# Optimization experiments

Measured on AMD Instinct MI355X. Metric: run time of the kernel, lower is better.

Reference implementation:

```python
import jax, jax.numpy as jnp
import numpy as np

GAMMA_MIN, GAMMA_MAX = 0.15, 1.0
ALPHA_CAP = 1.0
EPS_L2 = 1e-8
EPS_RMS = 1e-6


def _rmsnorm(x, w):
    return x * jax.lax.rsqrt(jnp.mean(x * x, axis=-1, keepdims=True) + EPS_RMS) * w


def _l2norm(x):
    n = jnp.linalg.norm(x, axis=-1, keepdims=True)
    return x / jnp.maximum(n, EPS_L2)


def _causal_conv(h, kernel):
    # depthwise-shared causal conv over time: out[b,t] = sum_j kernel[j] * h[b, t-j]
    K = kernel.shape[0]
    S = h.shape[1]
    hp = jnp.pad(h, ((0, 0), (K - 1, 0), (0, 0)))
    out = jnp.zeros_like(h)
    for j in range(K):  # K is a small fixed constant (4)
        out = out + kernel[j] * hp[:, K - 1 - j:K - 1 - j + S, :]
    return out


def setup_inputs() -> dict:
    B, S, D, R, K = 8, 1024, 1024, 16, 4
    key = jax.random.key(0)
    ks = jax.random.split(key, 8)
    return {
        'h': jax.random.normal(ks[0], (B, S, D), dtype=jnp.float32),
        'u': jax.random.normal(ks[1], (D, R), dtype=jnp.float32) * 0.05,
        'v': jax.random.normal(ks[2], (D, R), dtype=jnp.float32) * 0.05,
        'decay_logit': jnp.zeros((R,), jnp.float32),
        'alpha_logit': jnp.zeros((R,), jnp.float32),
        'k_base_gate_logit': jnp.float32(0.0),
        'k_base_kernel': jax.random.normal(ks[3], (K,), dtype=jnp.float32) * 0.05,
        'proj_w': jax.random.normal(ks[4], (D, D), dtype=jnp.float32) * 0.02,
        'proj_b': jnp.zeros((D,), jnp.float32),
        'norm1_w': jnp.ones((D,), jnp.float32),
        'norm2_w': jnp.ones((D,), jnp.float32),
        'mlp_w1': jax.random.normal(ks[5], (D, 4 * D), dtype=jnp.float32) * 0.02,
        'mlp_b1': jnp.zeros((4 * D,), jnp.float32),
        'mlp_w2': jax.random.normal(ks[6], (4 * D, D), dtype=jnp.float32) * 0.02,
        'mlp_b2': jnp.zeros((D,), jnp.float32),
    }


def reference(h, u, v, decay_logit, alpha_logit, k_base_gate_logit, k_base_kernel,
              proj_w, proj_b, norm1_w, norm2_w, mlp_w1, mlp_b1, mlp_w2, mlp_b2):
    B, S, D = h.shape
    R = u.shape[1]
    residual = h
    h_norm = _rmsnorm(h, norm1_w)

    # conv k_base term, gated
    gate = jax.nn.sigmoid(k_base_gate_logit)
    out = gate * _causal_conv(h_norm, k_base_kernel)

    # low-rank q/k projections
    alpha = ALPHA_CAP * jax.nn.sigmoid(alpha_logit)  # [R]
    qk = h_norm @ jnp.concatenate((u, v), axis=1)    # [B,S,2R]
    q_raw, k_raw = qk[..., :R], qk[..., R:]
    q = _l2norm(q_raw)
    k = _l2norm(k_raw)

    # per-rank causal decay matrix: w[r,i,j] = gamma[r]^(i-j) for i>=j else 0
    gamma = jnp.clip(jax.nn.sigmoid(decay_logit), GAMMA_MIN, GAMMA_MAX)  # [R]
    pos = jnp.arange(S, dtype=h.dtype)
    diff = jnp.maximum(pos[:, None] - pos[None, :], 0.0)   # [S,S]
    mask = jnp.tril(jnp.ones((S, S), dtype=h.dtype))
    w = (gamma[:, None, None] ** diff) * mask              # [R,S,S]

    q_alpha = q * alpha                                    # [B,S,R]
    A = jnp.einsum('bir,bjr,rij->bij', q_alpha, k, w)      # [B,S,S]
    decay_out = jnp.einsum('bij,bjd->bid', A, h_norm)      # [B,S,D]

    out = out + decay_out
    out = out @ proj_w.T + proj_b
    h2 = residual + out
    hn2 = _rmsnorm(h2, norm2_w)
    mlp_out = jax.nn.gelu(hn2 @ mlp_w1 + mlp_b1) @ mlp_w2 + mlp_b2
    return h2 + mlp_out
```

## Files before the change

### kernel.cpp

```cpp
#include <hip/hip_runtime.h>
#include <hip/hip_bf16.h>
#include <cstdint>
#include <cstddef>

typedef __bf16 bf16;
typedef __bf16 bf16x2 __attribute__((ext_vector_type(2)));
typedef __bf16 bf16x4 __attribute__((ext_vector_type(4)));
typedef __bf16 bf16x8 __attribute__((ext_vector_type(8)));
typedef float  floatx4 __attribute__((ext_vector_type(4)));

#define BB 8
#define SS 1024
#define DD 1024
#define RR 16
#define CHK 64
#define NCH 16

#define PP_ALPHA 0
#define PP_GAMMA 16
#define PP_GP    32
#define PP_KKER  (32 + 16*72)
#define PP_FLOATS 2048

__device__ __forceinline__ float sigmoidf_(float x) { return 1.0f / (1.0f + __expf(-x)); }

__device__ __forceinline__ float gelu_f(float x) {
    float u = 0.7978845608028654f * (x + 0.044715f * x * x * x);
    float t = 1.0f - 2.0f / (__expf(2.0f * u) + 1.0f);
    return 0.5f * x * (1.0f + t);
}

__device__ __forceinline__ void g2l16(const bf16* g, bf16* l) {
    __builtin_amdgcn_global_load_lds(
        (const __attribute__((address_space(1))) void*)g,
        (__attribute__((address_space(3))) void*)l, 16, 0, 0);
}

__global__ void params_kernel(const float* __restrict__ decay_logit,
                              const float* __restrict__ alpha_logit,
                              const float* __restrict__ gate_logit,
                              const float* __restrict__ kbase,
                              float* __restrict__ pp) {
    int t = threadIdx.x;
    if (t < 16) {
        pp[PP_ALPHA + t] = sigmoidf_(alpha_logit[t]);
        float g = sigmoidf_(decay_logit[t]);
        g = fminf(fmaxf(g, 0.15f), 1.0f);
        pp[PP_GAMMA + t] = g;
        float acc = 1.0f;
        for (int p = 0; p < 72; ++p) { pp[PP_GP + t * 72 + p] = acc; acc *= g; }
    }
    if (t >= 16 && t < 20) {
        float gate = sigmoidf_(gate_logit[0]);
        pp[PP_KKER + (t - 16)] = gate * kbase[t - 16];
    }
}

__global__ void uvt_kernel(const float* __restrict__ u, const float* __restrict__ v,
                           bf16* __restrict__ Ut) {
    int c = blockIdx.x;
    const float* src = (c < 16) ? u : v;
    int cc = c & 15;
    for (int d = threadIdx.x; d < 1024; d += 256)
        Ut[c * 1024 + d] = (bf16)src[d * 16 + cc];
}

__global__ __launch_bounds__(256) void rmsrow_kernel(
    const float* __restrict__ x, const float* __restrict__ nw, bf16* __restrict__ y) {
    __shared__ float red[4];
    int t = threadIdx.x;
    size_t row = blockIdx.x;
    float4 hv = ((const float4*)(x + row * DD))[t];
    float ss = hv.x*hv.x + hv.y*hv.y + hv.z*hv.z + hv.w*hv.w;
    for (int m = 32; m; m >>= 1) ss += __shfl_xor(ss, m);
    if ((t & 63) == 0) red[t >> 6] = ss;
    __syncthreads();
    float tot = red[0] + red[1] + red[2] + red[3];
    float rinv = rsqrtf(tot * (1.0f / 1024.0f) + 1e-6f);
    float4 wv = ((const float4*)nw)[t];
    bf16x4 o = { (bf16)(hv.x * rinv * wv.x), (bf16)(hv.y * rinv * wv.y),
                 (bf16)(hv.z * rinv * wv.z), (bf16)(hv.w * rinv * wv.w) };
    ((bf16x4*)(y + row * DD))[t] = o;
}

__global__ __launch_bounds__(256) void qk_kernel(
    const bf16* __restrict__ hn, const bf16* __restrict__ Ut,
    const float* __restrict__ pp, float* __restrict__ qa, float* __restrict__ kk) {
    __shared__ __attribute__((aligned(16))) bf16 As[128 * 64];
    __shared__ __attribute__((aligned(16))) bf16 Bs[32 * 64];
    int tid = threadIdx.x, lane = tid & 63, wid = tid >> 6;
    int quad = lane >> 4, l16 = lane & 15;
    int m0 = blockIdx.x * 128;
    int wm = wid * 32;
    const bf16* Ap[4]; int lo[4];
    #pragma unroll
    for (int j = 0; j < 4; ++j) {
        int s = j * 256 + tid;
        int row = s >> 3, cc = s & 7;
        int gc = cc ^ (row & 7);
        Ap[j] = hn + (size_t)(m0 + row) * DD + gc * 8;
        lo[j] = s * 8;
    }
    int bs_row = tid >> 3, bs_cc = tid & 7;
    int bs_gc = bs_cc ^ (bs_row & 7);
    const bf16* Bp = Ut + (size_t)bs_row * DD + bs_gc * 8;
    int blo = tid * 8;
    floatx4 acc[2][2] = {};
    for (int kt = 0; kt < 1024; kt += 64) {
        #pragma unroll
        for (int j = 0; j < 4; ++j) g2l16(Ap[j] + kt, As + lo[j]);
        g2l16(Bp + kt, Bs + blo);
        __syncthreads();
        #pragma unroll
        for (int ks = 0; ks < 2; ++ks) {
            bf16x8 af[2], bfr[2];
            #pragma unroll
            for (int tm = 0; tm < 2; ++tm) {
                int row = wm + tm * 16 + l16;
                int cc = (ks * 4 + quad) ^ (row & 7);
                af[tm] = *(const bf16x8*)(As + row * 64 + cc * 8);
            }
            #pragma unroll
            for (int tn = 0; tn < 2; ++tn) {
                int row = tn * 16 + l16;
                int cc = (ks * 4 + quad) ^ (row & 7);
                bfr[tn] = *(const bf16x8*)(Bs + row * 64 + cc * 8);
            }
            #pragma unroll
            for (int tm = 0; tm < 2; ++tm)
                #pragma unroll
                for (int tn = 0; tn < 2; ++tn)
                    acc[tm][tn] = __builtin_amdgcn_mfma_f32_16x16x32_bf16(
                        af[tm], bfr[tn], acc[tm][tn], 0, 0, 0);
        }
        __syncthreads();
    }
    float alf = pp[PP_ALPHA + l16];
    #pragma unroll
    for (int tm = 0; tm < 2; ++tm) {
        #pragma unroll
        for (int tn = 0; tn < 2; ++tn) {
            float s2[4];
            #pragma unroll
            for (int r = 0; r < 4; ++r) s2[r] = acc[tm][tn][r] * acc[tm][tn][r];
            #pragma unroll
            for (int m = 1; m <= 8; m <<= 1)
                #pragma unroll
                for (int r = 0; r < 4; ++r) s2[r] += __shfl_xor(s2[r], m);
            #pragma unroll
            for (int r = 0; r < 4; ++r) {
                size_t row = m0 + wm + tm * 16 + quad * 4 + r;
                float den = fmaxf(sqrtf(s2[r]), 1e-8f);
                float nvl = acc[tm][tn][r] / den;
                if (tn == 0) qa[row * RR + l16] = nvl * alf;
                else         kk[row * RR + l16] = nvl;
            }
        }
    }
}

__global__ __launch_bounds__(256) void incr_kernel(
    const bf16* __restrict__ hn, const float* __restrict__ kk,
    const float* __restrict__ pp, float* __restrict__ Inc) {
    __shared__ __attribute__((aligned(16))) float wjr[64][16];
    int t = threadIdx.x;
    int bc = blockIdx.x;
    int d0 = blockIdx.y * 256 + t;
    size_t row0 = (size_t)bc * 64;
    for (int idx = t; idx < 1024; idx += 256) {
        int j = idx >> 4, r = idx & 15;
        wjr[j][r] = kk[(row0 + j) * RR + r] * pp[PP_GP + r * 72 + (63 - j)];
    }
    __syncthreads();
    float acc[16] = {};
    for (int j = 0; j < 64; ++j) {
        float x = (float)hn[(row0 + j) * DD + d0];
        const float4* w4 = (const float4*)wjr[j];
        float4 w0 = w4[0], w1 = w4[1], w2 = w4[2], w3 = w4[3];
        acc[0]  += w0.x * x; acc[1]  += w0.y * x; acc[2]  += w0.z * x; acc[3]  += w0.w * x;
        acc[4]  += w1.x * x; acc[5]  += w1.y * x; acc[6]  += w1.z * x; acc[7]  += w1.w * x;
        acc[8]  += w2.x * x; acc[9]  += w2.y * x; acc[10] += w2.z * x; acc[11] += w2.w * x;
        acc[12] += w3.x * x; acc[13] += w3.y * x; acc[14] += w3.z * x; acc[15] += w3.w * x;
    }
    float* outp = Inc + (size_t)bc * 16 * 1024 + d0;
    #pragma unroll
    for (int r = 0; r < 16; ++r) outp[r * 1024] = acc[r];
}

__global__ __launch_bounds__(256) void scan_kernel(
    const float* __restrict__ Inc, const float* __restrict__ pp,
    float* __restrict__ Sprev) {
    int gid = blockIdx.x * 256 + threadIdx.x;
    int b = gid >> 14, rd = gid & 16383;
    int r = rd >> 10;
    float gd = pp[PP_GP + r * 72 + 64];
    float s = 0.0f;
    for (int c = 0; c < 16; ++c) {
        size_t idx = ((size_t)(b * 16 + c) << 14) + rd;
        Sprev[idx] = s;
        s = s * gd + Inc[idx];
    }
}

#define XK 104
__global__ __launch_bounds__(256, 2) void phasec_kernel(
    const bf16* __restrict__ hn, const float* __restrict__ qa, const float* __restrict__ kk,
    const float* __restrict__ Sprev, const float* __restrict__ pp,
    bf16* __restrict__ outpre) {
    __shared__ __attribute__((aligned(16))) bf16 Xt[128][XK];
    __shared__ __attribute__((aligned(16))) bf16 Mb[64][XK];
    __shared__ __attribute__((aligned(16))) float qa_s[64][16];
    __shared__ __attribute__((aligned(16))) float kk_s[64][16];
    __shared__ __attribute__((aligned(16))) float gpt[65][16];
    __shared__ float kks[4];
    int t = threadIdx.x;
    int bc = blockIdx.x;
    int c = bc & 15;
    int dt = blockIdx.y * 128;
    size_t row0 = (size_t)bc * 64;
    for (int idx = t; idx < 1024; idx += 256) {
        int j = idx >> 4, r = idx & 15;
        qa_s[j][r] = qa[(row0 + j) * RR + r];
        kk_s[j][r] = kk[(row0 + j) * RR + r];
    }
    for (int idx = t; idx < 16 * 65; idx += 256) {
        int p = idx >> 4, r = idx & 15;
        gpt[p][r] = pp[PP_GP + r * 72 + p];
    }
    if (t < 4) kks[t] = pp[PP_KKER + t];
    for (int idx = t; idx < 64 * 32; idx += 256) {
        int j = idx >> 5, ch = idx & 31;
        bf16x4 hv = *(const bf16x4*)(hn + (row0 + j) * DD + dt + ch * 4);
        #pragma unroll
        for (int e = 0; e < 4; ++e) Xt[ch * 4 + e][j] = hv[e];
    }
    for (int idx = t; idx < 16 * 128; idx += 256) {
        int r = idx >> 7, dd = idx & 127;
        Xt[dd][64 + r] = (bf16)Sprev[((size_t)bc << 14) + r * 1024 + dt + dd];
    }
    for (int idx = t; idx < 128 * 16; idx += 256) {
        int dd = idx >> 4, p = idx & 15;
        bf16 val = (bf16)0.0f;
        if (p < 3 && c > 0) val = hn[(row0 - 3 + p) * DD + dt + dd];
        Xt[dd][80 + p] = val;
    }
    __syncthreads();
    for (int idx = t; idx < 64 * 96; idx += 256) {
        int ii = idx / 96, jj = idx - ii * 96;
        float val = 0.0f;
        if (jj < 64) {
            if (jj <= ii) {
                const float4* qa4 = (const float4*)qa_s[ii];
                const float4* kk4 = (const float4*)kk_s[jj];
                const float4* gp4 = (const float4*)gpt[ii - jj];
                float s = 0.0f;
                #pragma unroll
                for (int x = 0; x < 4; ++x) {
                    float4 qv = qa4[x], kv = kk4[x], gv = gp4[x];
                    s += qv.x*kv.x*gv.x + qv.y*kv.y*gv.y + qv.z*kv.z*gv.z + qv.w*kv.w*gv.w;
                }
                val = s;
                if (ii - jj <= 3) val += kks[ii - jj];
            }
        } else if (jj < 80) {
            int r = jj - 64;
            val = qa_s[ii][r] * gpt[ii + 1][r];
        } else if (jj < 83) {
            int p = jj - 80;
            if (ii <= p) val = kks[ii + 3 - p];
        }
        Mb[ii][jj] = (bf16)val;
    }
    __syncthreads();
    int lane = t & 63, w = t >> 6;
    int quad = lane >> 4, l16 = lane & 15;
    floatx4 acc[8] = {};
    #pragma unroll
    for (int ks = 0; ks < 3; ++ks) {
        bf16x8 af = *(const bf16x8*)(&Mb[w * 16 + l16][ks * 32 + quad * 8]);
        #pragma unroll
        for (int tn = 0; tn < 8; ++tn) {
            bf16x8 bfr = *(const bf16x8*)(&Xt[tn * 16 + l16][ks * 32 + quad * 8]);
            acc[tn] = __builtin_amdgcn_mfma_f32_16x16x32_bf16(af, bfr, acc[tn], 0, 0, 0);
        }
    }
    #pragma unroll
    for (int tn = 0; tn < 8; ++tn) {
        #pragma unroll
        for (int r = 0; r < 4; ++r) {
            size_t ii = w * 16 + quad * 4 + r;
            outpre[(row0 + ii) * DD + dt + tn * 16 + l16] = (bf16)acc[tn][r];
        }
    }
}

__global__ void cvt_bf16_kernel(const float* __restrict__ in, bf16* __restrict__ out, int n4) {
    int i = blockIdx.x * 256 + threadIdx.x;
    if (i < n4) {
        float4 v = ((const float4*)in)[i];
        bf16x4 o = { (bf16)v.x, (bf16)v.y, (bf16)v.z, (bf16)v.w };
        ((bf16x4*)out)[i] = o;
    }
}

__global__ __launch_bounds__(256) void trcvt_kernel(
    const float* __restrict__ in, bf16* __restrict__ out, int K, int N) {
    __shared__ float tl[32][33];
    int x0 = blockIdx.x * 32, y0 = blockIdx.y * 32;
    int tx = threadIdx.x & 31, ty = threadIdx.x >> 5;
    #pragma unroll
    for (int i = 0; i < 4; ++i)
        tl[ty + i * 8][tx] = in[(size_t)(y0 + ty + i * 8) * N + x0 + tx];
    __syncthreads();
    #pragma unroll
    for (int i = 0; i < 4; ++i)
        out[(size_t)(x0 + ty + i * 8) * K + y0 + tx] = (bf16)tl[tx][ty + i * 8];
}

template <int EPI, int BK>
__global__ __launch_bounds__(256, 2) void gemm_bt_kernel(
    const bf16* __restrict__ A, const bf16* __restrict__ Bt,
    const float* __restrict__ bias, const float* __restrict__ resid,
    float* __restrict__ outf, bf16* __restrict__ outb, int K, int N) {
    constexpr int CH = BK / 8;
    constexpr int PT = 128 * CH / 256;
    __shared__ __attribute__((aligned(16))) bf16 As[128 * BK];
    __shared__ __attribute__((aligned(16))) bf16 Bs[128 * BK];
    int tid = threadIdx.x, lane = tid & 63, wid = tid >> 6;
    int quad = lane >> 4, l16 = lane & 15;
    int lb = blockIdx.y * gridDim.x + blockIdx.x;
    int xcd = lb & 7, q = lb >> 3;
    int m0 = (xcd * 8 + (q & 7)) * 128;
    int n0 = (q >> 3) * 128;
    int wm = (wid >> 1) * 64, wn = (wid & 1) * 64;
    const bf16* Ap[PT]; const bf16* Bp[PT]; int lo[PT];
    #pragma unroll
    for (int j = 0; j < PT; ++j) {
        int s = j * 256 + tid;
        int row = s / CH, cc = s % CH;
        int gc = cc ^ (row & (CH - 1));
        Ap[j] = A  + (size_t)(m0 + row) * K + gc * 8;
        Bp[j] = Bt + (size_t)(n0 + row) * K + gc * 8;
        lo[j] = s * 8;
    }
    floatx4 acc[4][4] = {};
    for (int kt = 0; kt < K; kt += BK) {
        #pragma unroll
        for (int j = 0; j < PT; ++j) {
            g2l16(Ap[j] + kt, As + lo[j]);
            g2l16(Bp[j] + kt, Bs + lo[j]);
        }
        __syncthreads();
        #pragma unroll
        for (int ks = 0; ks < BK / 32; ++ks) {
            bf16x8 af[4], bfr[4];
            #pragma unroll
            for (int tm = 0; tm < 4; ++tm) {
                int row = wm + tm * 16 + l16;
                int cc = (ks * 4 + quad) ^ (row & (CH - 1));
                af[tm] = *(const bf16x8*)(As + row * BK + cc * 8);
            }
            #pragma unroll
            for (int tn = 0; tn < 4; ++tn) {
                int row = wn + tn * 16 + l16;
                int cc = (ks * 4 + quad) ^ (row & (CH - 1));
                bfr[tn] = *(const bf16x8*)(Bs + row * BK + cc * 8);
            }
            #pragma unroll
            for (int tm = 0; tm < 4; ++tm)
                #pragma unroll
                for (int tn = 0; tn < 4; ++tn)
                    acc[tm][tn] = __builtin_amdgcn_mfma_f32_16x16x32_bf16(
                        af[tm], bfr[tn], acc[tm][tn], 0, 0, 0);
        }
        __syncthreads();
    }
    #pragma unroll
    for (int tn = 0; tn < 4; ++tn) {
        int gn = n0 + wn + tn * 16 + l16;
        float bs = bias[gn];
        #pragma unroll
        for (int tm = 0; tm < 4; ++tm) {
            #pragma unroll
            for (int r = 0; r < 4; ++r) {
                size_t gm = (size_t)m0 + wm + tm * 16 + quad * 4 + r;
                float v = acc[tm][tn][r] + bs;
                if (EPI == 1) {
                    outb[gm * N + gn] = (bf16)gelu_f(v);
                } else {
                    v += resid[gm * N + gn];
                    outf[gm * N + gn] = v;
                }
            }
        }
    }
}

extern "C" void kernel_launch(void* const* d_in, const int* in_sizes, int n_in,
                              void* d_out, int out_size, void* d_ws, size_t ws_size,
                              hipStream_t stream) {
    const float* h           = (const float*)d_in[0];
    const float* u           = (const float*)d_in[1];
    const float* v           = (const float*)d_in[2];
    const float* decay_logit = (const float*)d_in[3];
    const float* alpha_logit = (const float*)d_in[4];
    const float* gate_logit  = (const float*)d_in[5];
    const float* kbase       = (const float*)d_in[6];
    const float* proj_w      = (const float*)d_in[7];
    const float* proj_b      = (const float*)d_in[8];
    const float* norm1_w     = (const float*)d_in[9];
    const float* norm2_w     = (const float*)d_in[10];
    const float* mlp_w1      = (const float*)d_in[11];
    const float* mlp_b1      = (const float*)d_in[12];
    const float* mlp_w2      = (const float*)d_in[13];
    const float* mlp_b2      = (const float*)d_in[14];
    float* out = (float*)d_out;

    char* wsb = (char*)d_ws;
    size_t off = 0;
    auto alloc = [&](size_t bytes) -> void* {
        void* p = wsb + off;
        off += (bytes + 255) & ~(size_t)255;
        return p;
    };
    float* pp     = (float*)alloc(PP_FLOATS * 4);
    bf16*  Ut     = (bf16*) alloc((size_t)32 * 1024 * 2);
    bf16*  hn     = (bf16*) alloc((size_t)8192 * 1024 * 2);
    float* qa     = (float*)alloc((size_t)8192 * 16 * 4);
    float* kk     = (float*)alloc((size_t)8192 * 16 * 4);
    float* Inc    = (float*)alloc((size_t)128 * 16 * 1024 * 4);
    float* Sprev  = (float*)alloc((size_t)128 * 16 * 1024 * 4);
    bf16*  outpre = (bf16*) alloc((size_t)8192 * 1024 * 2);
    float* h2     = (float*)alloc((size_t)8192 * 1024 * 4);
    bf16*  hidden = (bf16*) alloc((size_t)8192 * 4096 * 2);
    bf16*  Wp     = (bf16*) alloc((size_t)1024 * 1024 * 2);
    bf16*  W1t    = (bf16*) alloc((size_t)4096 * 1024 * 2);
    bf16*  W2t    = (bf16*) alloc((size_t)1024 * 4096 * 2);
    bf16*  hn2 = hn;

    params_kernel<<<1, 64, 0, stream>>>(decay_logit, alpha_logit, gate_logit, kbase, pp);
    uvt_kernel<<<32, 256, 0, stream>>>(u, v, Ut);
    cvt_bf16_kernel<<<1024, 256, 0, stream>>>(proj_w, Wp, 1024 * 1024 / 4);
    trcvt_kernel<<<dim3(4096 / 32, 1024 / 32), 256, 0, stream>>>(mlp_w1, W1t, 1024, 4096);
    trcvt_kernel<<<dim3(1024 / 32, 4096 / 32), 256, 0, stream>>>(mlp_w2, W2t, 4096, 1024);
    rmsrow_kernel<<<8192, 256, 0, stream>>>(h, norm1_w, hn);
    qk_kernel<<<64, 256, 0, stream>>>(hn, Ut, pp, qa, kk);
    incr_kernel<<<dim3(128, 4), 256, 0, stream>>>(hn, kk, pp, Inc);
    scan_kernel<<<512, 256, 0, stream>>>(Inc, pp, Sprev);
    phasec_kernel<<<dim3(128, 8), 256, 0, stream>>>(hn, qa, kk, Sprev, pp, outpre);
    gemm_bt_kernel<0, 128><<<dim3(8, 64), 256, 0, stream>>>(outpre, Wp, proj_b, h, h2, nullptr, 1024, 1024);
    rmsrow_kernel<<<8192, 256, 0, stream>>>(h2, norm2_w, hn2);
    gemm_bt_kernel<1, 64><<<dim3(32, 64), 256, 0, stream>>>(hn2, W1t, mlp_b1, nullptr, nullptr, hidden, 1024, 4096);
    gemm_bt_kernel<2, 128><<<dim3(8, 64), 256, 0, stream>>>(hidden, W2t, mlp_b2, h2, out, nullptr, 4096, 1024);
}
```

Measured before the change: 394.1 us.

## Merge weight-prep kernels, retile qk, widen incr, reuse phasec mask across tiles

```diff
diff --git a/kernel.cpp b/kernel.cpp
--- a/kernel.cpp
+++ b/kernel.cpp
@@ -36,33 +36,67 @@
         (__attribute__((address_space(3))) void*)l, 16, 0, 0);
 }
 
-__global__ void params_kernel(const float* __restrict__ decay_logit,
-                              const float* __restrict__ alpha_logit,
-                              const float* __restrict__ gate_logit,
-                              const float* __restrict__ kbase,
-                              float* __restrict__ pp) {
+__global__ __launch_bounds__(256) void prep_kernel(
+    const float* __restrict__ decay_logit, const float* __restrict__ alpha_logit,
+    const float* __restrict__ gate_logit,  const float* __restrict__ kbase,
+    const float* __restrict__ u, const float* __restrict__ v,
+    const float* __restrict__ proj_w, const float* __restrict__ mlp_w1,
+    const float* __restrict__ mlp_w2,
+    float* __restrict__ pp, bf16* __restrict__ Ut, bf16* __restrict__ Wp,
+    bf16* __restrict__ W1t, bf16* __restrict__ W2t) {
+    __shared__ float tl[64][69];
     int t = threadIdx.x;
-    if (t < 16) {
-        pp[PP_ALPHA + t] = sigmoidf_(alpha_logit[t]);
-        float g = sigmoidf_(decay_logit[t]);
-        g = fminf(fmaxf(g, 0.15f), 1.0f);
-        pp[PP_GAMMA + t] = g;
-        float acc = 1.0f;
-        for (int p = 0; p < 72; ++p) { pp[PP_GP + t * 72 + p] = acc; acc *= g; }
-    }
-    if (t >= 16 && t < 20) {
-        float gate = sigmoidf_(gate_logit[0]);
-        pp[PP_KKER + (t - 16)] = gate * kbase[t - 16];
-    }
-}
-
-__global__ void uvt_kernel(const float* __restrict__ u, const float* __restrict__ v,
-                           bf16* __restrict__ Ut) {
-    int c = blockIdx.x;
-    const float* src = (c < 16) ? u : v;
-    int cc = c & 15;
-    for (int d = threadIdx.x; d < 1024; d += 256)
-        Ut[c * 1024 + d] = (bf16)src[d * 16 + cc];
+    int bid = blockIdx.x;
+    if (bid == 0) {
+        if (t < 16) {
+            pp[PP_ALPHA + t] = sigmoidf_(alpha_logit[t]);
+            float g = sigmoidf_(decay_logit[t]);
+            g = fminf(fmaxf(g, 0.15f), 1.0f);
+            pp[PP_GAMMA + t] = g;
+            float acc = 1.0f;
+            for (int p = 0; p < 72; ++p) { pp[PP_GP + t * 72 + p] = acc; acc *= g; }
+        }
+        if (t >= 16 && t < 20) {
+            float gate = sigmoidf_(gate_logit[0]);
+            pp[PP_KKER + (t - 16)] = gate * kbase[t - 16];
+        }
+        return;
+    }
+    if (bid < 33) {
+        int c = bid - 1;
+        const float* src = (c < 16) ? u : v;
+        int cc = c & 15;
+        for (int d = t; d < 1024; d += 256)
+            Ut[c * 1024 + d] = (bf16)src[d * 16 + cc];
+        return;
+    }
+    if (bid < 1057) {
+        int i = (bid - 33) * 256 + t;
+        float4 w = ((const float4*)proj_w)[i];
+        bf16x4 o = { (bf16)w.x, (bf16)w.y, (bf16)w.z, (bf16)w.w };
+        ((bf16x4*)Wp)[i] = o;
+        return;
+    }
+    const float* in; bf16* outp; int K, N, tb;
+    if (bid < 2081) { in = mlp_w1; outp = W1t; K = 1024; N = 4096; tb = bid - 1057; }
+    else            { in = mlp_w2; outp = W2t; K = 4096; N = 1024; tb = bid - 2081; }
+    int nx = N >> 6;
+    int x0 = (tb % nx) * 64, y0 = (tb / nx) * 64;
+    int tx = t & 15, ty = t >> 4;
+    #pragma unroll
+    for (int i = 0; i < 4; ++i) {
+        float4 w = *(const float4*)(in + (size_t)(y0 + ty + i * 16) * N + x0 + tx * 4);
+        tl[ty + i * 16][tx * 4 + 0] = w.x; tl[ty + i * 16][tx * 4 + 1] = w.y;
+        tl[ty + i * 16][tx * 4 + 2] = w.z; tl[ty + i * 16][tx * 4 + 3] = w.w;
+    }
+    __syncthreads();
+    #pragma unroll
+    for (int i = 0; i < 4; ++i) {
+        int nl = ty + i * 16;
+        bf16x4 o = { (bf16)tl[tx * 4 + 0][nl], (bf16)tl[tx * 4 + 1][nl],
+                     (bf16)tl[tx * 4 + 2][nl], (bf16)tl[tx * 4 + 3][nl] };
+        *(bf16x4*)(outp + (size_t)(x0 + nl) * K + y0 + tx * 4) = o;
+    }
 }
 
 __global__ __launch_bounds__(256) void rmsrow_kernel(
@@ -86,76 +120,49 @@
 __global__ __launch_bounds__(256) void qk_kernel(
     const bf16* __restrict__ hn, const bf16* __restrict__ Ut,
     const float* __restrict__ pp, float* __restrict__ qa, float* __restrict__ kk) {
-    __shared__ __attribute__((aligned(16))) bf16 As[128 * 64];
+    __shared__ __attribute__((aligned(16))) bf16 As[32 * 64];
     __shared__ __attribute__((aligned(16))) bf16 Bs[32 * 64];
     int tid = threadIdx.x, lane = tid & 63, wid = tid >> 6;
     int quad = lane >> 4, l16 = lane & 15;
-    int m0 = blockIdx.x * 128;
-    int wm = wid * 32;
-    const bf16* Ap[4]; int lo[4];
-    #pragma unroll
-    for (int j = 0; j < 4; ++j) {
-        int s = j * 256 + tid;
-        int row = s >> 3, cc = s & 7;
-        int gc = cc ^ (row & 7);
-        Ap[j] = hn + (size_t)(m0 + row) * DD + gc * 8;
-        lo[j] = s * 8;
-    }
-    int bs_row = tid >> 3, bs_cc = tid & 7;
-    int bs_gc = bs_cc ^ (bs_row & 7);
-    const bf16* Bp = Ut + (size_t)bs_row * DD + bs_gc * 8;
-    int blo = tid * 8;
-    floatx4 acc[2][2] = {};
+    int m0 = blockIdx.x * 32;
+    int mt = wid >> 1, nt = wid & 1;
+    int s_row = tid >> 3, s_cc = tid & 7;
+    int s_gc = s_cc ^ (s_row & 7);
+    const bf16* Ap = hn + (size_t)(m0 + s_row) * DD + s_gc * 8;
+    const bf16* Bp = Ut + (size_t)s_row * DD + s_gc * 8;
+    int slo = tid * 8;
+    floatx4 acc = {};
     for (int kt = 0; kt < 1024; kt += 64) {
-        #pragma unroll
-        for (int j = 0; j < 4; ++j) g2l16(Ap[j] + kt, As + lo[j]);
-        g2l16(Bp + kt, Bs + blo);
+        g2l16(Ap + kt, As + slo);
+        g2l16(Bp + kt, Bs + slo);
         __syncthreads();
         #pragma unroll
         for (int ks = 0; ks < 2; ++ks) {
-            bf16x8 af[2], bfr[2];
-            #pragma unroll
-            for (int tm = 0; tm < 2; ++tm) {
-                int row = wm + tm * 16 + l16;
-                int cc = (ks * 4 + quad) ^ (row & 7);
-                af[tm] = *(const bf16x8*)(As + row * 64 + cc * 8);
-            }
-            #pragma unroll
-            for (int tn = 0; tn < 2; ++tn) {
-                int row = tn * 16 + l16;
-                int cc = (ks * 4 + quad) ^ (row & 7);
-                bfr[tn] = *(const bf16x8*)(Bs + row * 64 + cc * 8);
-            }
-            #pragma unroll
-            for (int tm = 0; tm < 2; ++tm)
-                #pragma unroll
-                for (int tn = 0; tn < 2; ++tn)
-                    acc[tm][tn] = __builtin_amdgcn_mfma_f32_16x16x32_bf16(
-                        af[tm], bfr[tn], acc[tm][tn], 0, 0, 0);
+            int arow = mt * 16 + l16;
+            int acc_ = (ks * 4 + quad) ^ (arow & 7);
+            bf16x8 af = *(const bf16x8*)(As + arow * 64 + acc_ * 8);
+            int brow = nt * 16 + l16;
+            int bcc = (ks * 4 + quad) ^ (brow & 7);
+            bf16x8 bfr = *(const bf16x8*)(Bs + brow * 64 + bcc * 8);
+            acc = __builtin_amdgcn_mfma_f32_16x16x32_bf16(af, bfr, acc, 0, 0, 0);
         }
         __syncthreads();
     }
     float alf = pp[PP_ALPHA + l16];
-    #pragma unroll
-    for (int tm = 0; tm < 2; ++tm) {
-        #pragma unroll
-        for (int tn = 0; tn < 2; ++tn) {
-            float s2[4];
-            #pragma unroll
-            for (int r = 0; r < 4; ++r) s2[r] = acc[tm][tn][r] * acc[tm][tn][r];
-            #pragma unroll
-            for (int m = 1; m <= 8; m <<= 1)
-                #pragma unroll
-                for (int r = 0; r < 4; ++r) s2[r] += __shfl_xor(s2[r], m);
-            #pragma unroll
-            for (int r = 0; r < 4; ++r) {
-                size_t row = m0 + wm + tm * 16 + quad * 4 + r;
-                float den = fmaxf(sqrtf(s2[r]), 1e-8f);
-                float nvl = acc[tm][tn][r] / den;
-                if (tn == 0) qa[row * RR + l16] = nvl * alf;
-                else         kk[row * RR + l16] = nvl;
-            }
-        }
+    float s2[4];
+    #pragma unroll
+    for (int r = 0; r < 4; ++r) s2[r] = acc[r] * acc[r];
+    #pragma unroll
+    for (int m = 1; m <= 8; m <<= 1)
+        #pragma unroll
+        for (int r = 0; r < 4; ++r) s2[r] += __shfl_xor(s2[r], m);
+    #pragma unroll
+    for (int r = 0; r < 4; ++r) {
+        size_t row = m0 + mt * 16 + quad * 4 + r;
+        float den = fmaxf(sqrtf(s2[r]), 1e-8f);
+        float nvl = acc[r] / den;
+        if (nt == 0) qa[row * RR + l16] = nvl * alf;
+        else         kk[row * RR + l16] = nvl;
     }
 }
 
@@ -165,26 +172,33 @@
     __shared__ __attribute__((aligned(16))) float wjr[64][16];
     int t = threadIdx.x;
     int bc = blockIdx.x;
-    int d0 = blockIdx.y * 256 + t;
+    int d0 = blockIdx.y * 512 + t * 2;
     size_t row0 = (size_t)bc * 64;
     for (int idx = t; idx < 1024; idx += 256) {
         int j = idx >> 4, r = idx & 15;
         wjr[j][r] = kk[(row0 + j) * RR + r] * pp[PP_GP + r * 72 + (63 - j)];
     }
     __syncthreads();
-    float acc[16] = {};
+    float acc0[16] = {}, acc1[16] = {};
     for (int j = 0; j < 64; ++j) {
-        float x = (float)hn[(row0 + j) * DD + d0];
+        bf16x2 hv = *(const bf16x2*)(hn + (row0 + j) * DD + d0);
+        float x0 = (float)hv[0], x1 = (float)hv[1];
         const float4* w4 = (const float4*)wjr[j];
-        float4 w0 = w4[0], w1 = w4[1], w2 = w4[2], w3 = w4[3];
-        acc[0]  += w0.x * x; acc[1]  += w0.y * x; acc[2]  += w0.z * x; acc[3]  += w0.w * x;
-        acc[4]  += w1.x * x; acc[5]  += w1.y * x; acc[6]  += w1.z * x; acc[7]  += w1.w * x;
-        acc[8]  += w2.x * x; acc[9]  += w2.y * x; acc[10] += w2.z * x; acc[11] += w2.w * x;
-        acc[12] += w3.x * x; acc[13] += w3.y * x; acc[14] += w3.z * x; acc[15] += w3.w * x;
+        #pragma unroll
+        for (int g = 0; g < 4; ++g) {
+            float4 w = w4[g];
+            acc0[g*4+0] += w.x * x0; acc0[g*4+1] += w.y * x0;
+            acc0[g*4+2] += w.z * x0; acc0[g*4+3] += w.w * x0;
+            acc1[g*4+0] += w.x * x1; acc1[g*4+1] += w.y * x1;
+            acc1[g*4+2] += w.z * x1; acc1[g*4+3] += w.w * x1;
+        }
     }
     float* outp = Inc + (size_t)bc * 16 * 1024 + d0;
     #pragma unroll
-    for (int r = 0; r < 16; ++r) outp[r * 1024] = acc[r];
+    for (int r = 0; r < 16; ++r) {
+        float2 o = { acc0[r], acc1[r] };
+        *(float2*)&outp[r * 1024] = o;
+    }
 }
 
 __global__ __launch_bounds__(256) void scan_kernel(
@@ -216,7 +230,6 @@
     int t = threadIdx.x;
     int bc = blockIdx.x;
     int c = bc & 15;
-    int dt = blockIdx.y * 128;
     size_t row0 = (size_t)bc * 64;
     for (int idx = t; idx < 1024; idx += 256) {
         int j = idx >> 4, r = idx & 15;
@@ -228,22 +241,6 @@
         gpt[p][r] = pp[PP_GP + r * 72 + p];
     }
     if (t < 4) kks[t] = pp[PP_KKER + t];
-    for (int idx = t; idx < 64 * 32; idx += 256) {
-        int j = idx >> 5, ch = idx & 31;
-        bf16x4 hv = *(const bf16x4*)(hn + (row0 + j) * DD + dt + ch * 4);
-        #pragma unroll
-        for (int e = 0; e < 4; ++e) Xt[ch * 4 + e][j] = hv[e];
-    }
-    for (int idx = t; idx < 16 * 128; idx += 256) {
-        int r = idx >> 7, dd = idx & 127;
-        Xt[dd][64 + r] = (bf16)Sprev[((size_t)bc << 14) + r * 1024 + dt + dd];
-    }
-    for (int idx = t; idx < 128 * 16; idx += 256) {
-        int dd = idx >> 4, p = idx & 15;
-        bf16 val = (bf16)0.0f;
-        if (p < 3 && c > 0) val = hn[(row0 - 3 + p) * DD + dt + dd];
-        Xt[dd][80 + p] = val;
-    }
     __syncthreads();
     for (int idx = t; idx < 64 * 96; idx += 256) {
         int ii = idx / 96, jj = idx - ii * 96;
@@ -271,50 +268,49 @@
         }
         Mb[ii][jj] = (bf16)val;
     }
-    __syncthreads();
-    int lane = t & 63, w = t >> 6;
-    int quad = lane >> 4, l16 = lane & 15;
-    floatx4 acc[8] = {};
-    #pragma unroll
-    for (int ks = 0; ks < 3; ++ks) {
-        bf16x8 af = *(const bf16x8*)(&Mb[w * 16 + l16][ks * 32 + quad * 8]);
+    int lane = t & 63, w = t >> 6, quad = lane >> 4, l16 = lane & 15;
+    for (int it = 0; it < 2; ++it) {
+        int dt = blockIdx.y * 256 + it * 128;
+        __syncthreads();
+        for (int idx = t; idx < 64 * 32; idx += 256) {
+            int j = idx >> 5, ch = idx & 31;
+            bf16x4 hv = *(const bf16x4*)(hn + (row0 + j) * DD + dt + ch * 4);
+            #pragma unroll
+            for (int ee = 0; ee < 4; ++ee) {
+                int e = (ee + t) & 3;
+                Xt[ch * 4 + e][j] = hv[e];
+            }
+        }
+        for (int idx = t; idx < 16 * 128; idx += 256) {
+            int r = idx >> 7, dd = idx & 127;
+            Xt[dd][64 + r] = (bf16)Sprev[((size_t)bc << 14) + r * 1024 + dt + dd];
+        }
+        for (int idx = t; idx < 128 * 16; idx += 256) {
+            int dd = idx >> 4, p = idx & 15;
+            bf16 val = (bf16)0.0f;
+            if (p < 3 && c > 0) val = hn[(row0 - 3 + p) * DD + dt + dd];
+            Xt[dd][80 + p] = val;
+        }
+        __syncthreads();
+        floatx4 acc[8] = {};
+        #pragma unroll
+        for (int ks = 0; ks < 3; ++ks) {
+            bf16x8 af = *(const bf16x8*)(&Mb[w * 16 + l16][ks * 32 + quad * 8]);
+            #pragma unroll
+            for (int tn = 0; tn < 8; ++tn) {
+                bf16x8 bfr = *(const bf16x8*)(&Xt[tn * 16 + l16][ks * 32 + quad * 8]);
+                acc[tn] = __builtin_amdgcn_mfma_f32_16x16x32_bf16(af, bfr, acc[tn], 0, 0, 0);
+            }
+        }
         #pragma unroll
         for (int tn = 0; tn < 8; ++tn) {
-            bf16x8 bfr = *(const bf16x8*)(&Xt[tn * 16 + l16][ks * 32 + quad * 8]);
-            acc[tn] = __builtin_amdgcn_mfma_f32_16x16x32_bf16(af, bfr, acc[tn], 0, 0, 0);
-        }
-    }
-    #pragma unroll
-    for (int tn = 0; tn < 8; ++tn) {
-        #pragma unroll
-        for (int r = 0; r < 4; ++r) {
-            size_t ii = w * 16 + quad * 4 + r;
-            outpre[(row0 + ii) * DD + dt + tn * 16 + l16] = (bf16)acc[tn][r];
-        }
-    }
-}
-
-__global__ void cvt_bf16_kernel(const float* __restrict__ in, bf16* __restrict__ out, int n4) {
-    int i = blockIdx.x * 256 + threadIdx.x;
-    if (i < n4) {
-        float4 v = ((const float4*)in)[i];
-        bf16x4 o = { (bf16)v.x, (bf16)v.y, (bf16)v.z, (bf16)v.w };
-        ((bf16x4*)out)[i] = o;
-    }
-}
-
-__global__ __launch_bounds__(256) void trcvt_kernel(
-    const float* __restrict__ in, bf16* __restrict__ out, int K, int N) {
-    __shared__ float tl[32][33];
-    int x0 = blockIdx.x * 32, y0 = blockIdx.y * 32;
-    int tx = threadIdx.x & 31, ty = threadIdx.x >> 5;
-    #pragma unroll
-    for (int i = 0; i < 4; ++i)
-        tl[ty + i * 8][tx] = in[(size_t)(y0 + ty + i * 8) * N + x0 + tx];
-    __syncthreads();
-    #pragma unroll
-    for (int i = 0; i < 4; ++i)
-        out[(size_t)(x0 + ty + i * 8) * K + y0 + tx] = (bf16)tl[tx][ty + i * 8];
+            #pragma unroll
+            for (int r = 0; r < 4; ++r) {
+                size_t ii = w * 16 + quad * 4 + r;
+                outpre[(row0 + ii) * DD + dt + tn * 16 + l16] = (bf16)acc[tn][r];
+            }
+        }
+    }
 }
 
 template <int EPI, int BK>
@@ -438,16 +434,14 @@
     bf16*  W2t    = (bf16*) alloc((size_t)1024 * 4096 * 2);
     bf16*  hn2 = hn;
 
-    params_kernel<<<1, 64, 0, stream>>>(decay_logit, alpha_logit, gate_logit, kbase, pp);
-    uvt_kernel<<<32, 256, 0, stream>>>(u, v, Ut);
-    cvt_bf16_kernel<<<1024, 256, 0, stream>>>(proj_w, Wp, 1024 * 1024 / 4);
-    trcvt_kernel<<<dim3(4096 / 32, 1024 / 32), 256, 0, stream>>>(mlp_w1, W1t, 1024, 4096);
-    trcvt_kernel<<<dim3(1024 / 32, 4096 / 32), 256, 0, stream>>>(mlp_w2, W2t, 4096, 1024);
+    prep_kernel<<<3105, 256, 0, stream>>>(decay_logit, alpha_logit, gate_logit, kbase,
+                                          u, v, proj_w, mlp_w1, mlp_w2,
+                                          pp, Ut, Wp, W1t, W2t);
     rmsrow_kernel<<<8192, 256, 0, stream>>>(h, norm1_w, hn);
-    qk_kernel<<<64, 256, 0, stream>>>(hn, Ut, pp, qa, kk);
-    incr_kernel<<<dim3(128, 4), 256, 0, stream>>>(hn, kk, pp, Inc);
+    qk_kernel<<<256, 256, 0, stream>>>(hn, Ut, pp, qa, kk);
+    incr_kernel<<<dim3(128, 2), 256, 0, stream>>>(hn, kk, pp, Inc);
     scan_kernel<<<512, 256, 0, stream>>>(Inc, pp, Sprev);
-    phasec_kernel<<<dim3(128, 8), 256, 0, stream>>>(hn, qa, kk, Sprev, pp, outpre);
+    phasec_kernel<<<dim3(128, 4), 256, 0, stream>>>(hn, qa, kk, Sprev, pp, outpre);
     gemm_bt_kernel<0, 128><<<dim3(8, 64), 256, 0, stream>>>(outpre, Wp, proj_b, h, h2, nullptr, 1024, 1024);
     rmsrow_kernel<<<8192, 256, 0, stream>>>(h2, norm2_w, hn2);
     gemm_bt_kernel<1, 64><<<dim3(32, 64), 256, 0, stream>>>(hn2, W1t, mlp_b1, nullptr, nullptr, hidden, 1024, 4096);
```

New measurement: 374.8 us. -4.9%, faster.
